# Kernel tuning notes

Hardware: AMD Instinct MI355X
Metric: run time of the kernel (lower is better)

## Reference

```python
import jax, jax.numpy as jnp
import numpy as np

B, N, J, D, H = 64, 128, 512, 1024, 4096
ITERS, EPS = 3, 1e-8
SCALE = D ** -0.5
LN_EPS = 1e-5  # torch LayerNorm default


def _ln(x, g, b):
    m = jnp.mean(x, axis=-1, keepdims=True)
    v = jnp.mean((x - m) ** 2, axis=-1, keepdims=True)
    return (x - m) * jax.lax.rsqrt(v + LN_EPS) * g + b


def setup_inputs() -> dict:
    key = jax.random.key(0)
    ks = jax.random.split(key, 24)
    p = lambda i, shape: jax.random.normal(ks[i], shape, jnp.float32) * 0.02
    return {
        "inputs": jax.random.normal(ks[0], (B, N, D), jnp.float32),
        "texts": jax.random.normal(ks[1], (J, D), jnp.float32),
        "Wq": p(2, (D, D)), "bq": jnp.zeros((D,), jnp.float32),
        "Wk": p(3, (D, D)), "bk": jnp.zeros((D,), jnp.float32),
        "Wv": p(4, (D, D)), "bv": jnp.zeros((D,), jnp.float32),
        "W_ih": p(5, (3 * D, D)), "b_ih": jnp.zeros((3 * D,), jnp.float32),
        "W_hh": p(6, (3 * D, D)), "b_hh": jnp.zeros((3 * D,), jnp.float32),
        "W1": p(7, (H, D)), "b1": jnp.zeros((H,), jnp.float32),
        "W2": p(8, (D, H)), "b2": jnp.zeros((D,), jnp.float32),
        "g_in": jnp.ones((D,), jnp.float32), "be_in": jnp.zeros((D,), jnp.float32),
        "g_sl": jnp.ones((D,), jnp.float32), "be_sl": jnp.zeros((D,), jnp.float32),
        "g_ff": jnp.ones((D,), jnp.float32), "be_ff": jnp.zeros((D,), jnp.float32),
    }


def reference(inputs, texts, Wq, bq, Wk, bk, Wv, bv, W_ih, b_ih, W_hh, b_hh,
              W1, b1, W2, b2, g_in, be_in, g_sl, be_sl, g_ff, be_ff):
    slots = inputs                                  # [B, N, D]
    texts_n = _ln(texts, g_in, be_in)               # [J, D] (repeat == broadcast)
    k = texts_n @ Wk.T + bk                         # [J, D]
    v = texts_n @ Wv.T + bv                         # [J, D]
    for _ in range(ITERS):
        slots_prev = slots
        q = _ln(slots, g_sl, be_sl) @ Wq.T + bq     # [B, N, D]
        dots = jnp.einsum('bid,jd->bij', q, k) * SCALE
        attn = jax.nn.softmax(dots, axis=1) + EPS   # softmax over slots dim
        attn = attn / jnp.sum(attn, axis=-1, keepdims=True)
        updates = jnp.einsum('jd,bij->bid', v, attn)
        # GRUCell: input=updates, hidden=slots_prev (torch gate order r, z, n)
        gi = updates @ W_ih.T + b_ih
        gh = slots_prev @ W_hh.T + b_hh
        i_r, i_z, i_n = jnp.split(gi, 3, axis=-1)
        h_r, h_z, h_n = jnp.split(gh, 3, axis=-1)
        r = jax.nn.sigmoid(i_r + h_r)
        z = jax.nn.sigmoid(i_z + h_z)
        n = jnp.tanh(i_n + r * h_n)
        slots = (1.0 - z) * n + z * slots_prev
        ff = _ln(slots, g_ff, be_ff)
        slots = slots + (jax.nn.relu(ff @ W1.T + b1) @ W2.T + b2)
    return slots
```

## Files before the change

### kernel.cpp

```cpp
#include <hip/hip_runtime.h>
#include <hip/hip_bf16.h>
#include <stdint.h>


using bf16 = __hip_bfloat16;
typedef __bf16 bf16x8 __attribute__((ext_vector_type(8)));
typedef float f32x4 __attribute__((ext_vector_type(4)));

#define F_RELU    1
#define F_SIGMOID 2
#define F_EPSC    8

__device__ __forceinline__ void gl_to_lds16(const void* g, void* l) {
  __builtin_amdgcn_global_load_lds(
      (const __attribute__((address_space(1))) uint32_t*)(uintptr_t)g,
      (__attribute__((address_space(3))) uint32_t*)(uintptr_t)l,
      16, 0, 0);
}

template <int BN>
__global__ __launch_bounds__(256, 4) void gemm_bt(
    const bf16* __restrict__ X, int ldx,
    const bf16* __restrict__ W, int ldw,
    const float* __restrict__ bias,
    int M, int N, int K, float scale, int flags,
    float* __restrict__ outF, int ldf,
    bf16* __restrict__ outB, int ldb,
    const float* __restrict__ resid,
    const float* __restrict__ auxA,
    const float* __restrict__ auxB)
{
  constexpr int NJ = BN / 32;
  __shared__ __align__(16) bf16 As[128 * 64];
  __shared__ __align__(16) bf16 Bs[BN * 64];
  const int t = threadIdx.x;
  const int m0 = blockIdx.x * 128, n0 = blockIdx.y * BN;
  const int wave = t >> 6, lane = t & 63;
  const int wm = (wave >> 1) * 64, wn = (wave & 1) * (BN / 2);
  const int lrow = lane & 15, quad = lane >> 4;

  f32x4 acc[4][NJ] = {};

  const int srow = t >> 3;
  const int scol = ((t & 7) ^ (srow & 7)) * 8;
  const bf16* Ag = X + (size_t)(m0 + srow) * ldx + scol;
  const bf16* Bg = W + (size_t)(n0 + srow) * ldw + scol;
  bf16* Al = As + t * 8;
  bf16* Bl = Bs + t * 8;

  const int r3 = lrow & 7;
  const int c0 = quad ^ r3;
  const int c1 = (4 + quad) ^ r3;

  for (int k0 = 0; k0 < K; k0 += 64) {
#pragma unroll
    for (int u = 0; u < 4; ++u)
      gl_to_lds16(Ag + k0 + (size_t)(u * 32) * ldx, Al + u * 2048);
#pragma unroll
    for (int u = 0; u < NJ; ++u)
      gl_to_lds16(Bg + k0 + (size_t)(u * 32) * ldw, Bl + u * 2048);
    __syncthreads();
    const bf16x8* AS = (const bf16x8*)As;
    const bf16x8* BS = (const bf16x8*)Bs;
#pragma unroll
    for (int kk = 0; kk < 2; ++kk) {
      const int ck = kk ? c1 : c0;
      bf16x8 af[4], bfr[NJ];
#pragma unroll
      for (int i = 0; i < 4; i++)  af[i]  = AS[(wm + i * 16 + lrow) * 8 + ck];
#pragma unroll
      for (int j = 0; j < NJ; j++) bfr[j] = BS[(wn + j * 16 + lrow) * 8 + ck];
#pragma unroll
      for (int i = 0; i < 4; i++)
#pragma unroll
        for (int j = 0; j < NJ; j++)
          acc[i][j] = __builtin_amdgcn_mfma_f32_16x16x32_bf16(af[i], bfr[j], acc[i][j], 0, 0, 0);
    }
    __syncthreads();
  }

#pragma unroll
  for (int i = 0; i < 4; i++) {
    const int row0 = m0 + wm + i * 16 + quad * 4;
#pragma unroll
    for (int j = 0; j < NJ; j++) {
      const int col = n0 + wn + j * 16 + lrow;
      const float badd = bias ? bias[col] : 0.f;
#pragma unroll
      for (int r = 0; r < 4; r++) {
        const int row = row0 + r;
        float val = acc[i][j][r] * scale + badd;
        if (flags & F_EPSC)    val += 1e-8f * auxA[col] * auxB[row];
        if (flags & F_RELU)    val = fmaxf(val, 0.f);
        if (flags & F_SIGMOID) val = 1.f / (1.f + expf(-val));
        if (resid) val += resid[(size_t)row * ldf + col];
        if (outF) outF[(size_t)row * ldf + col] = val;
        if (outB) outB[(size_t)row * ldb + col] = __float2bfloat16(val);
      }
    }
  }
}

__global__ __launch_bounds__(256, 4) void gemm_gru(
    const bf16* __restrict__ X,
    const bf16* __restrict__ Wc,
    const float* __restrict__ bihn,
    const float* __restrict__ bhhn,
    const float* __restrict__ cn,
    const float* __restrict__ rinv,
    const bf16* __restrict__ rz,
    float* __restrict__ slots)
{
  __shared__ __align__(16) bf16 As[128 * 64];
  __shared__ __align__(16) bf16 Bs[64 * 64];
  const int t = threadIdx.x;
  const int m0 = blockIdx.x * 128, n0 = blockIdx.y * 64;
  const int wave = t >> 6, lane = t & 63;
  const int wm = (wave >> 1) * 64, wn = (wave & 1) * 32;
  const int lrow = lane & 15, quad = lane >> 4;

  f32x4 accN[4][2] = {};
  f32x4 accH[4][2] = {};

  const int srow = t >> 3;
  const int scol = ((t & 7) ^ (srow & 7)) * 8;
  const bf16* Ag = X + (size_t)(m0 + srow) * 1536 + scol;
  const bf16* Bg = Wc + (size_t)(n0 + srow) * 1536 + scol;
  bf16* Al = As + t * 8;
  bf16* Bl = Bs + t * 8;

  const int r3 = lrow & 7;
  const int c0 = quad ^ r3;
  const int c1 = (4 + quad) ^ r3;

  for (int k0 = 0; k0 < 512; k0 += 64) {
#pragma unroll
    for (int u = 0; u < 4; ++u)
      gl_to_lds16(Ag + k0 + (size_t)(u * 32) * 1536, Al + u * 2048);
#pragma unroll
    for (int u = 0; u < 2; ++u)
      gl_to_lds16(Bg + k0 + (size_t)(u * 32) * 1536, Bl + u * 2048);
    __syncthreads();
    const bf16x8* AS = (const bf16x8*)As;
    const bf16x8* BS = (const bf16x8*)Bs;
#pragma unroll
    for (int kk = 0; kk < 2; ++kk) {
      const int ck = kk ? c1 : c0;
      bf16x8 af[4], bfr[2];
#pragma unroll
      for (int i = 0; i < 4; i++) af[i] = AS[(wm + i * 16 + lrow) * 8 + ck];
#pragma unroll
      for (int j = 0; j < 2; j++) bfr[j] = BS[(wn + j * 16 + lrow) * 8 + ck];
#pragma unroll
      for (int i = 0; i < 4; i++)
#pragma unroll
        for (int j = 0; j < 2; j++)
          accN[i][j] = __builtin_amdgcn_mfma_f32_16x16x32_bf16(af[i], bfr[j], accN[i][j], 0, 0, 0);
    }
    __syncthreads();
  }
  for (int k0 = 512; k0 < 1536; k0 += 64) {
#pragma unroll
    for (int u = 0; u < 4; ++u)
      gl_to_lds16(Ag + k0 + (size_t)(u * 32) * 1536, Al + u * 2048);
#pragma unroll
    for (int u = 0; u < 2; ++u)
      gl_to_lds16(Bg + k0 + (size_t)(u * 32) * 1536, Bl + u * 2048);
    __syncthreads();
    const bf16x8* AS = (const bf16x8*)As;
    const bf16x8* BS = (const bf16x8*)Bs;
#pragma unroll
    for (int kk = 0; kk < 2; ++kk) {
      const int ck = kk ? c1 : c0;
      bf16x8 af[4], bfr[2];
#pragma unroll
      for (int i = 0; i < 4; i++) af[i] = AS[(wm + i * 16 + lrow) * 8 + ck];
#pragma unroll
      for (int j = 0; j < 2; j++) bfr[j] = BS[(wn + j * 16 + lrow) * 8 + ck];
#pragma unroll
      for (int i = 0; i < 4; i++)
#pragma unroll
        for (int j = 0; j < 2; j++)
          accH[i][j] = __builtin_amdgcn_mfma_f32_16x16x32_bf16(af[i], bfr[j], accH[i][j], 0, 0, 0);
    }
    __syncthreads();
  }

#pragma unroll
  for (int i = 0; i < 4; i++) {
    const int row0 = m0 + wm + i * 16 + quad * 4;
#pragma unroll
    for (int j = 0; j < 2; j++) {
      const int col = n0 + wn + j * 16 + lrow;
      const float bN = bihn[col] + 1e-8f * cn[col] * 0.f;
      const float bH = bhhn[col];
      const float cc = cn[col];
#pragma unroll
      for (int r = 0; r < 4; r++) {
        const int row = row0 + r;
        const size_t ridx = (size_t)row * 1024 + col;
        const float vn = accN[i][j][r] + bN + 1e-8f * cc * rinv[row];
        const float vh = accH[i][j][r] + bH;
        const float rg = __bfloat162float(rz[(size_t)row * 2048 + col]);
        const float zg = __bfloat162float(rz[(size_t)row * 2048 + 1024 + col]);
        const float ng = tanhf(vn + rg * vh);
        const float prev = slots[ridx];
        slots[ridx] = (1.f - zg) * ng + zg * prev;
      }
    }
  }
}

__global__ __launch_bounds__(256) void ln_rows(const float* __restrict__ x,
    const float* __restrict__ g, const float* __restrict__ b,
    bf16* __restrict__ out, int ldo)
{
  const int row = blockIdx.x;
  const int t = threadIdx.x;
  const float* xr = x + (size_t)row * 1024;
  float v[4];
  float s = 0.f, s2 = 0.f;
#pragma unroll
  for (int i = 0; i < 4; i++) {
    float val = xr[t + 256 * i];
    v[i] = val; s += val; s2 += val * val;
  }
#pragma unroll
  for (int off = 32; off > 0; off >>= 1) {
    s  += __shfl_down(s, off);
    s2 += __shfl_down(s2, off);
  }
  __shared__ float rs[4], rs2[4];
  if ((t & 63) == 0) { rs[t >> 6] = s; rs2[t >> 6] = s2; }
  __syncthreads();
  const float S  = rs[0] + rs[1] + rs[2] + rs[3];
  const float S2 = rs2[0] + rs2[1] + rs2[2] + rs2[3];
  const float mean = S * (1.f / 1024.f);
  const float var  = S2 * (1.f / 1024.f) - mean * mean;
  const float rstd = rsqrtf(var + 1e-5f);
  bf16* outr = out + (size_t)row * ldo;
#pragma unroll
  for (int i = 0; i < 4; i++) {
    const int c = t + 256 * i;
    outr[c] = __float2bfloat16((v[i] - mean) * rstd * g[c] + b[c]);
  }
}

__global__ __launch_bounds__(256) void softmax_fused(
    const float* __restrict__ dots, bf16* __restrict__ xcat2,
    float* __restrict__ P)
{
  __shared__ float tile[128][65];
  __shared__ float cred[4][64];
  __shared__ float colmax[64], colinv[64];
  const int b = blockIdx.x, jt = blockIdx.y;
  const int t = threadIdx.x;
  const float* src = dots + (size_t)b * (128 * 512) + jt * 64;
#pragma unroll
  for (int p = 0; p < 32; p++) {
    const int i = p * 4 + (t >> 6), c = t & 63;
    tile[i][c] = src[(size_t)i * 512 + c];
  }
  __syncthreads();
  const int c = t & 63, s = t >> 6;
  float mx = -1e30f;
  for (int i = s * 32; i < s * 32 + 32; i++) mx = fmaxf(mx, tile[i][c]);
  cred[s][c] = mx;
  __syncthreads();
  if (s == 0) colmax[c] = fmaxf(fmaxf(cred[0][c], cred[1][c]),
                                fmaxf(cred[2][c], cred[3][c]));
  __syncthreads();
  const float cm = colmax[c];
  float sum = 0.f;
  for (int i = s * 32; i < s * 32 + 32; i++) {
    const float e = expf(tile[i][c] - cm);
    tile[i][c] = e; sum += e;
  }
  cred[s][c] = sum;
  __syncthreads();
  if (s == 0) colinv[c] = 1.f / (cred[0][c] + cred[1][c] + cred[2][c] + cred[3][c]);
  __syncthreads();
  bf16* dst = xcat2 + (size_t)b * 128 * 1536 + jt * 64;
#pragma unroll
  for (int p = 0; p < 32; p++) {
    const int i = p * 4 + (t >> 6), cc = t & 63;
    dst[(size_t)i * 1536 + cc] = __float2bfloat16(tile[i][cc] * colinv[cc]);
  }
  if (t < 128) {
    float rs = 0.f;
    for (int cc = 0; cc < 64; cc++) rs += tile[t][cc] * colinv[cc];
    P[((size_t)b * 128 + t) * 8 + jt] = rs;
  }
}

__global__ __launch_bounds__(256) void rowinv_k(const float* __restrict__ P,
                                                float* __restrict__ rowinv)
{
  const int m = blockIdx.x * 256 + threadIdx.x;
  const float* p = P + (size_t)m * 8;
  float s = 0.f;
#pragma unroll
  for (int i = 0; i < 8; i++) s += p[i];
  rowinv[m] = 1.f / (s + 512.f * 1e-8f);
}

__global__ __launch_bounds__(256) void smscale(bf16* __restrict__ x,
                                               const float* __restrict__ rinv)
{
  const int idx = blockIdx.x * 256 + threadIdx.x;
  const int m = idx >> 9, j = idx & 511;
  const size_t a = (size_t)m * 1536 + j;
  x[a] = __float2bfloat16(__bfloat162float(x[a]) * rinv[m]);
}

__global__ __launch_bounds__(256) void init_slots(const float* __restrict__ x,
    float* __restrict__ sf, bf16* __restrict__ xr)
{
  const size_t base = (size_t)blockIdx.x * 1024 + threadIdx.x;
#pragma unroll
  for (int i = 0; i < 4; i++) {
    const size_t idx = base + 256 * i;
    const float v = x[idx];
    sf[idx] = v;
    xr[(idx >> 10) * 1536 + (idx & 1023)] = __float2bfloat16(v);
  }
}

__global__ __launch_bounds__(256) void f2b(const float* __restrict__ x,
                                           bf16* __restrict__ y)
{
  const size_t base = (size_t)blockIdx.x * 1024 + threadIdx.x;
#pragma unroll
  for (int i = 0; i < 4; i++) y[base + 256 * i] = __float2bfloat16(x[base + 256 * i]);
}

__global__ __launch_bounds__(256) void f2b_ld(const float* __restrict__ src,
                                              bf16* __restrict__ dst, int dstld)
{
  const int idx = blockIdx.x * 256 + threadIdx.x;
  const int n = idx >> 10, c = idx & 1023;
  dst[(size_t)n * dstld + c] = __float2bfloat16(src[(size_t)n * 1024 + c]);
}

__global__ __launch_bounds__(256) void f2b_T(const float* __restrict__ Wq,
                                             bf16* __restrict__ wqT)
{
  const int idx = blockIdx.x * 256 + threadIdx.x;
  const int d = idx >> 10, dp = idx & 1023;
  wqT[idx] = __float2bfloat16(Wq[(size_t)dp * 1024 + d]);
}

__global__ __launch_bounds__(256) void make_brz(const float* __restrict__ bih,
    const float* __restrict__ bhh, float* __restrict__ brz)
{
  const int n = blockIdx.x * 256 + threadIdx.x;
  brz[n] = bih[n] + bhh[n];
}

__global__ __launch_bounds__(256) void make_bqk(const bf16* __restrict__ k,
    const float* __restrict__ bq, float* __restrict__ bqk, float scale)
{
  const int j = blockIdx.x * 256 + threadIdx.x;
  const bf16* kr = k + (size_t)j * 1024;
  float s = 0.f;
  for (int d = 0; d < 1024; d++) s += bq[d] * __bfloat162float(kr[d]);
  bqk[j] = scale * s;
}

__global__ __launch_bounds__(256) void make_vcol(const bf16* __restrict__ v,
                                                 float* __restrict__ vcol)
{
  const int d = blockIdx.x * 256 + threadIdx.x;
  float s = 0.f;
  for (int j = 0; j < 512; j++) s += __bfloat162float(v[(size_t)j * 1024 + d]);
  vcol[d] = s;
}

__global__ __launch_bounds__(256) void make_c(const float* __restrict__ Wih,
    const float* __restrict__ vcol, float* __restrict__ c)
{
  const int n = blockIdx.x;
  const int t = threadIdx.x;
  const float* wr = Wih + (size_t)n * 1024;
  float s = 0.f;
#pragma unroll
  for (int i = 0; i < 4; i++) s += wr[t + 256 * i] * vcol[t + 256 * i];
#pragma unroll
  for (int off = 32; off > 0; off >>= 1) s += __shfl_down(s, off);
  __shared__ float rs[4];
  if ((t & 63) == 0) rs[t >> 6] = s;
  __syncthreads();
  if (t == 0) c[n] = rs[0] + rs[1] + rs[2] + rs[3];
}

extern "C" void kernel_launch(void* const* d_in, const int* in_sizes, int n_in,
                              void* d_out, int out_size, void* d_ws, size_t ws_size,
                              hipStream_t stream)
{
  const float* inputs = (const float*)d_in[0];
  const float* texts  = (const float*)d_in[1];
  const float* Wq  = (const float*)d_in[2];  const float* bq  = (const float*)d_in[3];
  const float* Wk  = (const float*)d_in[4];  const float* bk  = (const float*)d_in[5];
  const float* Wv  = (const float*)d_in[6];  const float* bv  = (const float*)d_in[7];
  const float* Wih = (const float*)d_in[8];  const float* bih = (const float*)d_in[9];
  const float* Whh = (const float*)d_in[10]; const float* bhh = (const float*)d_in[11];
  const float* W1  = (const float*)d_in[12]; const float* b1  = (const float*)d_in[13];
  const float* W2  = (const float*)d_in[14]; const float* b2  = (const float*)d_in[15];
  const float* g_in = (const float*)d_in[16]; const float* be_in = (const float*)d_in[17];
  const float* g_sl = (const float*)d_in[18]; const float* be_sl = (const float*)d_in[19];
  const float* g_ff = (const float*)d_in[20]; const float* be_ff = (const float*)d_in[21];

  constexpr int B = 64, N = 128, J = 512, D = 1024, H = 4096;
  constexpr int M = B * N;
  const float SCALE = 0.03125f;

  char* ws = (char*)d_ws;
  size_t off = 0;
  auto alloc = [&](size_t bytes) -> char* {
    char* p = ws + off; off += (bytes + 255) & ~(size_t)255; return p;
  };
  bf16* wk_b    = (bf16*)alloc((size_t)D * D * 2);
  bf16* wv_b    = (bf16*)alloc((size_t)D * D * 2);
  bf16* w1_b    = (bf16*)alloc((size_t)H * D * 2);
  bf16* w2_b    = (bf16*)alloc((size_t)D * H * 2);
  bf16* win_b   = (bf16*)alloc((size_t)D * D * 2);
  bf16* wihrz_b = (bf16*)alloc((size_t)2048 * D * 2);
  bf16* wqT_b   = (bf16*)alloc((size_t)D * D * 2);
  bf16* wcat2_b = (bf16*)alloc((size_t)2048 * 1536 * 2);
  bf16* ptnw_b  = (bf16*)alloc((size_t)D * 1536 * 2);
  bf16* kq_b    = (bf16*)alloc((size_t)J * D * 2);
  bf16* texts_n = (bf16*)alloc((size_t)J * D * 2);
  bf16* k_b     = (bf16*)alloc((size_t)J * D * 2);
  bf16* v_b     = (bf16*)alloc((size_t)J * D * 2);
  bf16* xcat2_b = (bf16*)alloc((size_t)M * 1536 * 2);
  float* brz_b  = (float*)alloc((size_t)2048 * 4);
  float* bqk_b  = (float*)alloc((size_t)J * 4);
  float* vcol_b = (float*)alloc((size_t)D * 4);
  float* c_b    = (float*)alloc((size_t)3072 * 4);
  float* P_b    = (float*)alloc((size_t)M * 8 * 4);
  float* rinv_b = (float*)alloc((size_t)M * 4);
  char* U = alloc((size_t)48 * 1024 * 1024);
  bf16*  xln_b  = (bf16*)(U);
  float* dots_f = (float*)(U + (size_t)16 * 1024 * 1024);
  bf16*  rz_b   = (bf16*)(U + (size_t)32 * 1024 * 1024);
  bf16*  h1_b   = (bf16*)(U + (size_t)16 * 1024 * 1024);
  rz_b = (bf16*)(U);

  if (ws_size < off) return;

  float* slots_f = (float*)d_out;

  f2b<<<dim3(D * D / 1024), 256, 0, stream>>>(Wk, wk_b);
  f2b<<<dim3(D * D / 1024), 256, 0, stream>>>(Wv, wv_b);
  f2b<<<dim3(H * D / 1024), 256, 0, stream>>>(W1, w1_b);
  f2b<<<dim3(D * H / 1024), 256, 0, stream>>>(W2, w2_b);
  f2b<<<dim3(D * D / 1024), 256, 0, stream>>>(Wih + (size_t)2048 * D, win_b);
  f2b<<<dim3(2048 * D / 1024), 256, 0, stream>>>(Wih, wihrz_b);
  f2b_T<<<dim3(D * D / 256), 256, 0, stream>>>(Wq, wqT_b);
  f2b_ld<<<dim3(2048 * 1024 / 256), 256, 0, stream>>>(Whh, wcat2_b + 512, 1536);
  f2b_ld<<<dim3(1024 * 1024 / 256), 256, 0, stream>>>(
      Whh + (size_t)2048 * D, ptnw_b + 512, 1536);
  make_brz<<<dim3(8), 256, 0, stream>>>(bih, bhh, brz_b);

  init_slots<<<dim3(M * D / 1024), 256, 0, stream>>>(inputs, slots_f, xcat2_b + 512);

  ln_rows<<<dim3(J), 256, 0, stream>>>(texts, g_in, be_in, texts_n, D);
  gemm_bt<64><<<dim3(J / 128, D / 64), 256, 0, stream>>>(
      texts_n, D, wk_b, D, bk, J, D, D, 1.f, 0,
      nullptr, 0, k_b, D, nullptr, nullptr, nullptr);
  gemm_bt<64><<<dim3(J / 128, D / 64), 256, 0, stream>>>(
      texts_n, D, wv_b, D, bv, J, D, D, 1.f, 0,
      nullptr, 0, v_b, D, nullptr, nullptr, nullptr);
  gemm_bt<64><<<dim3(J / 128, D / 64), 256, 0, stream>>>(
      k_b, D, wqT_b, D, nullptr, J, D, D, 1.f, 0,
      nullptr, 0, kq_b, D, nullptr, nullptr, nullptr);
  gemm_bt<64><<<dim3(2048 / 128, J / 64), 256, 0, stream>>>(
      wihrz_b, D, v_b, D, nullptr, 2048, J, D, 1.f, 0,
      nullptr, 0, wcat2_b, 1536, nullptr, nullptr, nullptr);
  gemm_bt<64><<<dim3(D / 128, J / 64), 256, 0, stream>>>(
      win_b, D, v_b, D, nullptr, D, J, D, 1.f, 0,
      nullptr, 0, ptnw_b, 1536, nullptr, nullptr, nullptr);
  make_bqk<<<dim3(2), 256, 0, stream>>>(k_b, bq, bqk_b, SCALE);
  make_vcol<<<dim3(4), 256, 0, stream>>>(v_b, vcol_b);
  make_c<<<dim3(3072), 256, 0, stream>>>(Wih, vcol_b, c_b);

  for (int it = 0; it < 3; it++) {
    ln_rows<<<dim3(M), 256, 0, stream>>>(slots_f, g_sl, be_sl, xln_b, D);
    gemm_bt<64><<<dim3(M / 128, J / 64), 256, 0, stream>>>(
        xln_b, D, kq_b, D, bqk_b, M, J, D, SCALE, 0,
        dots_f, J, nullptr, 0, nullptr, nullptr, nullptr);
    softmax_fused<<<dim3(B, 8), 256, 0, stream>>>(dots_f, xcat2_b, P_b);
    rowinv_k<<<dim3(M / 256), 256, 0, stream>>>(P_b, rinv_b);
    smscale<<<dim3(M * 512 / 256), 256, 0, stream>>>(xcat2_b, rinv_b);
    gemm_bt<128><<<dim3(M / 128, 2048 / 128), 256, 0, stream>>>(
        xcat2_b, 1536, wcat2_b, 1536, brz_b, M, 2048, 1536, 1.f, F_SIGMOID | F_EPSC,
        nullptr, 0, rz_b, 2048, nullptr, c_b, rinv_b);
    gemm_gru<<<dim3(M / 128, D / 64), 256, 0, stream>>>(
        xcat2_b, ptnw_b, bih + 2048, bhh + 2048, c_b + 2048, rinv_b,
        rz_b, slots_f);
    ln_rows<<<dim3(M), 256, 0, stream>>>(slots_f, g_ff, be_ff, xln_b, D);
    gemm_bt<128><<<dim3(M / 128, 2048 / 128), 256, 0, stream>>>(
        xln_b, D, w1_b, D, b1, M, 2048, D, 1.f, F_RELU,
        nullptr, 0, h1_b, 2048, nullptr, nullptr, nullptr);
    gemm_bt<64><<<dim3(M / 128, D / 64), 256, 0, stream>>>(
        h1_b, 2048, w2_b, H, b2, M, D, 2048, 1.f, 0,
        slots_f, D, nullptr, 0, slots_f, nullptr, nullptr);
    gemm_bt<128><<<dim3(M / 128, 2048 / 128), 256, 0, stream>>>(
        xln_b, D, w1_b + (size_t)2048 * D, D, b1 + 2048, M, 2048, D, 1.f, F_RELU,
        nullptr, 0, h1_b, 2048, nullptr, nullptr, nullptr);
    gemm_bt<64><<<dim3(M / 128, D / 64), 256, 0, stream>>>(
        h1_b, 2048, w2_b + 2048, H, nullptr, M, D, 2048, 1.f, 0,
        slots_f, D, xcat2_b + 512, 1536, slots_f, nullptr, nullptr);
  }
}
```

Baseline: 1.395 ms.

## Fuse dots GEMM with column softmax into one kernel via shared LDS tile

Replaces the separate dots GEMM plus softmax_fused pair with one kernel that computes the 128x64 dots tile with MFMA. It writes the tile into the same LDS buffer used for staging and runs the slot-dim softmax and row-partial sums in place. This removes the fp32 dots round trip through global memory and one launch per iteration. It also raises gemm_bt's launch-bounds occupancy hint from 4 to 5, which may constrain register allocation, and drops a no-op term in the GRU epilogue.

Result: slower. 1.879 ms (+34.7%).

```diff
diff --git a/kernel.cpp b/kernel.cpp
--- a/kernel.cpp
+++ b/kernel.cpp
@@ -19,7 +19,7 @@
 }
 
 template <int BN>
-__global__ __launch_bounds__(256, 4) void gemm_bt(
+__global__ __launch_bounds__(256, 5) void gemm_bt(
     const bf16* __restrict__ X, int ldx,
     const bf16* __restrict__ W, int ldw,
     const float* __restrict__ bias,
@@ -101,6 +101,110 @@
   }
 }
 
+__global__ __launch_bounds__(256, 4) void dots_sm(
+    const bf16* __restrict__ X,
+    const bf16* __restrict__ Wk,
+    const float* __restrict__ bqk,
+    float scale,
+    bf16* __restrict__ xcat2, float* __restrict__ P)
+{
+  __shared__ __align__(16) char usm[128 * 65 * 4];
+  __shared__ float cred[4][64];
+  __shared__ float colmax[64], colinv[64];
+  bf16* As = (bf16*)usm;
+  bf16* Bs = (bf16*)(usm + 16384);
+  const int t = threadIdx.x;
+  const int m0 = blockIdx.x * 128, n0 = blockIdx.y * 64;
+  const int wave = t >> 6, lane = t & 63;
+  const int wm = (wave >> 1) * 64, wn = (wave & 1) * 32;
+  const int lrow = lane & 15, quad = lane >> 4;
+
+  f32x4 acc[4][2] = {};
+
+  const int srow = t >> 3;
+  const int scol = ((t & 7) ^ (srow & 7)) * 8;
+  const bf16* Ag = X + (size_t)(m0 + srow) * 1024 + scol;
+  const bf16* Bg = Wk + (size_t)(n0 + srow) * 1024 + scol;
+  bf16* Al = As + t * 8;
+  bf16* Bl = Bs + t * 8;
+
+  const int r3 = lrow & 7;
+  const int c0 = quad ^ r3;
+  const int c1 = (4 + quad) ^ r3;
+
+  for (int k0 = 0; k0 < 1024; k0 += 64) {
+#pragma unroll
+    for (int u = 0; u < 4; ++u)
+      gl_to_lds16(Ag + k0 + (size_t)(u * 32) * 1024, Al + u * 2048);
+#pragma unroll
+    for (int u = 0; u < 2; ++u)
+      gl_to_lds16(Bg + k0 + (size_t)(u * 32) * 1024, Bl + u * 2048);
+    __syncthreads();
+    const bf16x8* AS = (const bf16x8*)As;
+    const bf16x8* BS = (const bf16x8*)Bs;
+#pragma unroll
+    for (int kk = 0; kk < 2; ++kk) {
+      const int ck = kk ? c1 : c0;
+      bf16x8 af[4], bfr[2];
+#pragma unroll
+      for (int i = 0; i < 4; i++) af[i] = AS[(wm + i * 16 + lrow) * 8 + ck];
+#pragma unroll
+      for (int j = 0; j < 2; j++) bfr[j] = BS[(wn + j * 16 + lrow) * 8 + ck];
+#pragma unroll
+      for (int i = 0; i < 4; i++)
+#pragma unroll
+        for (int j = 0; j < 2; j++)
+          acc[i][j] = __builtin_amdgcn_mfma_f32_16x16x32_bf16(af[i], bfr[j], acc[i][j], 0, 0, 0);
+    }
+    __syncthreads();
+  }
+
+  float (*tile)[65] = (float(*)[65])usm;
+#pragma unroll
+  for (int i = 0; i < 4; i++) {
+    const int rl0 = wm + i * 16 + quad * 4;
+#pragma unroll
+    for (int j = 0; j < 2; j++) {
+      const int cl = wn + j * 16 + lrow;
+      const float badd = bqk[n0 + cl];
+#pragma unroll
+      for (int r = 0; r < 4; r++)
+        tile[rl0 + r][cl] = acc[i][j][r] * scale + badd;
+    }
+  }
+  __syncthreads();
+
+  const int c = t & 63, s = t >> 6;
+  float mx = -1e30f;
+  for (int i = s * 32; i < s * 32 + 32; i++) mx = fmaxf(mx, tile[i][c]);
+  cred[s][c] = mx;
+  __syncthreads();
+  if (s == 0) colmax[c] = fmaxf(fmaxf(cred[0][c], cred[1][c]),
+                                fmaxf(cred[2][c], cred[3][c]));
+  __syncthreads();
+  const float cm = colmax[c];
+  float sum = 0.f;
+  for (int i = s * 32; i < s * 32 + 32; i++) {
+    const float e = expf(tile[i][c] - cm);
+    tile[i][c] = e; sum += e;
+  }
+  cred[s][c] = sum;
+  __syncthreads();
+  if (s == 0) colinv[c] = 1.f / (cred[0][c] + cred[1][c] + cred[2][c] + cred[3][c]);
+  __syncthreads();
+  bf16* dst = xcat2 + (size_t)blockIdx.x * 128 * 1536 + blockIdx.y * 64;
+#pragma unroll
+  for (int p = 0; p < 32; p++) {
+    const int i = p * 4 + (t >> 6), cc = t & 63;
+    dst[(size_t)i * 1536 + cc] = __float2bfloat16(tile[i][cc] * colinv[cc]);
+  }
+  if (t < 128) {
+    float rs = 0.f;
+    for (int cc = 0; cc < 64; cc++) rs += tile[t][cc] * colinv[cc];
+    P[((size_t)blockIdx.x * 128 + t) * 8 + blockIdx.y] = rs;
+  }
+}
+
 __global__ __launch_bounds__(256, 4) void gemm_gru(
     const bf16* __restrict__ X,
     const bf16* __restrict__ Wc,
@@ -192,7 +296,7 @@
 #pragma unroll
     for (int j = 0; j < 2; j++) {
       const int col = n0 + wn + j * 16 + lrow;
-      const float bN = bihn[col] + 1e-8f * cn[col] * 0.f;
+      const float bN = bihn[col];
       const float bH = bhhn[col];
       const float cc = cn[col];
 #pragma unroll
@@ -243,53 +347,6 @@
   for (int i = 0; i < 4; i++) {
     const int c = t + 256 * i;
     outr[c] = __float2bfloat16((v[i] - mean) * rstd * g[c] + b[c]);
-  }
-}
-
-__global__ __launch_bounds__(256) void softmax_fused(
-    const float* __restrict__ dots, bf16* __restrict__ xcat2,
-    float* __restrict__ P)
-{
-  __shared__ float tile[128][65];
-  __shared__ float cred[4][64];
-  __shared__ float colmax[64], colinv[64];
-  const int b = blockIdx.x, jt = blockIdx.y;
-  const int t = threadIdx.x;
-  const float* src = dots + (size_t)b * (128 * 512) + jt * 64;
-#pragma unroll
-  for (int p = 0; p < 32; p++) {
-    const int i = p * 4 + (t >> 6), c = t & 63;
-    tile[i][c] = src[(size_t)i * 512 + c];
-  }
-  __syncthreads();
-  const int c = t & 63, s = t >> 6;
-  float mx = -1e30f;
-  for (int i = s * 32; i < s * 32 + 32; i++) mx = fmaxf(mx, tile[i][c]);
-  cred[s][c] = mx;
-  __syncthreads();
-  if (s == 0) colmax[c] = fmaxf(fmaxf(cred[0][c], cred[1][c]),
-                                fmaxf(cred[2][c], cred[3][c]));
-  __syncthreads();
-  const float cm = colmax[c];
-  float sum = 0.f;
-  for (int i = s * 32; i < s * 32 + 32; i++) {
-    const float e = expf(tile[i][c] - cm);
-    tile[i][c] = e; sum += e;
-  }
-  cred[s][c] = sum;
-  __syncthreads();
-  if (s == 0) colinv[c] = 1.f / (cred[0][c] + cred[1][c] + cred[2][c] + cred[3][c]);
-  __syncthreads();
-  bf16* dst = xcat2 + (size_t)b * 128 * 1536 + jt * 64;
-#pragma unroll
-  for (int p = 0; p < 32; p++) {
-    const int i = p * 4 + (t >> 6), cc = t & 63;
-    dst[(size_t)i * 1536 + cc] = __float2bfloat16(tile[i][cc] * colinv[cc]);
-  }
-  if (t < 128) {
-    float rs = 0.f;
-    for (int cc = 0; cc < 64; cc++) rs += tile[t][cc] * colinv[cc];
-    P[((size_t)b * 128 + t) * 8 + jt] = rs;
   }
 }
 
@@ -441,10 +498,8 @@
   float* rinv_b = (float*)alloc((size_t)M * 4);
   char* U = alloc((size_t)48 * 1024 * 1024);
   bf16*  xln_b  = (bf16*)(U);
-  float* dots_f = (float*)(U + (size_t)16 * 1024 * 1024);
-  bf16*  rz_b   = (bf16*)(U + (size_t)32 * 1024 * 1024);
+  bf16*  rz_b   = (bf16*)(U);
   bf16*  h1_b   = (bf16*)(U + (size_t)16 * 1024 * 1024);
-  rz_b = (bf16*)(U);
 
   if (ws_size < off) return;
 
@@ -486,10 +541,8 @@
 
   for (int it = 0; it < 3; it++) {
     ln_rows<<<dim3(M), 256, 0, stream>>>(slots_f, g_sl, be_sl, xln_b, D);
-    gemm_bt<64><<<dim3(M / 128, J / 64), 256, 0, stream>>>(
-        xln_b, D, kq_b, D, bqk_b, M, J, D, SCALE, 0,
-        dots_f, J, nullptr, 0, nullptr, nullptr, nullptr);
-    softmax_fused<<<dim3(B, 8), 256, 0, stream>>>(dots_f, xcat2_b, P_b);
+    dots_sm<<<dim3(M / 128, J / 64), 256, 0, stream>>>(
+        xln_b, kq_b, bqk_b, SCALE, xcat2_b, P_b);
     rowinv_k<<<dim3(M / 256), 256, 0, stream>>>(P_b, rinv_b);
     smscale<<<dim3(M * 512 / 256), 256, 0, stream>>>(xcat2_b, rinv_b);
     gemm_bt<128><<<dim3(M / 128, 2048 / 128), 256, 0, stream>>>(
```
